# Performance work log

Measured on AMD Instinct MI355X. Metric: run time of the kernel, lower is better.

Reference implementation:

```python
import jax, jax.numpy as jnp
import numpy as np

GAMMA = 0.99
BETA = 0.01
B, T, A = 65536, 128, 8


def setup_inputs() -> dict:
    key = jax.random.key(0)
    ks = jax.random.split(key, 6)
    return {
        "values": jax.random.normal(ks[0], (B, T), jnp.float32),
        "last_value": jax.random.normal(ks[1], (B,), jnp.float32),
        "rewards": jax.random.normal(ks[2], (B, T), jnp.float32),
        "log_probs": -jax.nn.softplus(jax.random.normal(ks[3], (B, T, A), jnp.float32)),
        "entropies": jax.random.uniform(ks[4], (B, T, A), jnp.float32),
        "terminal_mask": jax.random.randint(ks[5], (B,), 0, 2) > 0,
    }


def _a3c_loss(values, last_value, rewards, log_probs, entropies, terminal_mask):
    # Bootstrap value R: zero if terminal, else detached last-state value
    R0 = jnp.where(terminal_mask, 0.0, jax.lax.stop_gradient(last_value))  # [B]
    values_next = jnp.concatenate([values[:, 1:], R0[:, None]], axis=1)    # [B,T] = values[i+1]
    lp = log_probs.sum(-1)    # [B,T], log_probs[i].sum()
    ent = entropies.sum(-1)   # [B,T], entropies[i].sum()

    # scan over time (reverse), xs laid out time-major: [T, B]
    xs = (rewards.T, values.T, values_next.T, lp.T, ent.T)
    z = jnp.zeros((values.shape[0],), values.dtype)

    def step(carry, x):
        R, gae, actor, critic = carry
        r, v, v_next, l, e = x
        R = GAMMA * R + r
        adv = R - v
        critic = critic + 0.5 * adv * adv
        delta = r + GAMMA * v_next - v
        gae = gae * GAMMA + delta
        actor = actor - l * jax.lax.stop_gradient(gae) - BETA * e
        return (R, gae, actor, critic), None

    (R, gae, actor, critic), _ = jax.lax.scan(step, (R0, z, z, z), xs, reverse=True)
    return jnp.stack([actor, critic], axis=-1)  # [B, 2]: (actor_loss, critic_loss)


def reference(values, last_value, rewards, log_probs, entropies, terminal_mask):
    return _a3c_loss(values, last_value, rewards, log_probs, entropies, terminal_mask)
```

## Files before the change

kernel.cpp:

```cpp
#include <hip/hip_runtime.h>

#define GAMMA 0.99f
#define BETA  0.01f

__global__ __launch_bounds__(256, 8) void a3c_loss_kernel(
    const float* __restrict__ values,
    const float* __restrict__ last_value,
    const float* __restrict__ rewards,
    const float* __restrict__ log_probs,
    const float* __restrict__ entropies,
    const int*   __restrict__ terminal_mask,
    float* __restrict__ out,
    int B)
{
    const int wave = threadIdx.x >> 6;
    const int lane = threadIdx.x & 63;
    const int b = blockIdx.x * 4 + wave;
    if (b >= B) return;

    const float2 v2 = reinterpret_cast<const float2*>(values  + (size_t)b * 128)[lane];
    const float2 r2 = reinterpret_cast<const float2*>(rewards + (size_t)b * 128)[lane];
    const float4* lp4 = reinterpret_cast<const float4*>(log_probs + (size_t)b * 1024) + lane * 4;
    const float4* en4 = reinterpret_cast<const float4*>(entropies + (size_t)b * 1024) + lane * 4;
    const float4 la = lp4[0], lb = lp4[1], lc = lp4[2], ld = lp4[3];
    const float4 ea = en4[0], eb = en4[1], ec = en4[2], ed = en4[3];

    const float v0 = v2.x, v1 = v2.y;
    const float r0 = r2.x, r1 = r2.y;
    const float lp0 = (la.x + la.y + la.z + la.w) + (lb.x + lb.y + lb.z + lb.w);
    const float lp1 = (lc.x + lc.y + lc.z + lc.w) + (ld.x + ld.y + ld.z + ld.w);
    const float esum = (ea.x + ea.y + ea.z + ea.w) + (eb.x + eb.y + eb.z + eb.w)
                     + (ec.x + ec.y + ec.z + ec.w) + (ed.x + ed.y + ed.z + ed.w);

    const float R0 = (terminal_mask[b] != 0) ? 0.0f : last_value[b];

    float vnext1 = __shfl_down(v0, 1, 64);
    if (lane == 63) vnext1 = R0;
    const float delta1 = r1 + GAMMA * vnext1 - v1;
    const float delta0 = r0 + GAMMA * v1    - v0;

    float m  = GAMMA * GAMMA;
    float cR = fmaf(GAMMA, r1, r0);
    float cG = fmaf(GAMMA, delta1, delta0);

    #pragma unroll
    for (int d = 1; d < 64; d <<= 1) {
        const float om  = __shfl_down(m,  d, 64);
        const float ocR = __shfl_down(cR, d, 64);
        const float ocG = __shfl_down(cG, d, 64);
        if (lane + d < 64) {
            cR = fmaf(m, ocR, cR);
            cG = fmaf(m, ocG, cG);
            m  = m * om;
        }
    }
    float pm  = __shfl_down(m,  1, 64);
    float pcR = __shfl_down(cR, 1, 64);
    float pcG = __shfl_down(cG, 1, 64);
    if (lane == 63) { pm = 1.0f; pcR = 0.0f; pcG = 0.0f; }

    const float Rin = fmaf(pm, R0, pcR);
    const float gin = pcG;

    const float R1   = fmaf(GAMMA, Rin, r1);
    const float Rt0  = fmaf(GAMMA, R1,  r0);
    const float adv1 = R1  - v1;
    const float adv0 = Rt0 - v0;
    float critic = 0.5f * (adv1 * adv1 + adv0 * adv0);

    const float g1 = fmaf(GAMMA, gin, delta1);
    const float g0 = fmaf(GAMMA, g1,  delta0);
    float actor = -(lp1 * g1 + lp0 * g0) - BETA * esum;

    #pragma unroll
    for (int d = 32; d >= 1; d >>= 1) {
        actor  += __shfl_down(actor,  d, 64);
        critic += __shfl_down(critic, d, 64);
    }

    if (lane == 0) {
        reinterpret_cast<float2*>(out)[b] = make_float2(actor, critic);
    }
}

extern "C" void kernel_launch(void* const* d_in, const int* in_sizes, int n_in,
                              void* d_out, int out_size, void* d_ws, size_t ws_size,
                              hipStream_t stream) {
    const float* values      = (const float*)d_in[0];
    const float* last_value  = (const float*)d_in[1];
    const float* rewards     = (const float*)d_in[2];
    const float* log_probs   = (const float*)d_in[3];
    const float* entropies   = (const float*)d_in[4];
    const int*   terminal    = (const int*)d_in[5];
    float* out = (float*)d_out;

    const int B = in_sizes[1];
    const int blocks = (B + 3) / 4;

    a3c_loss_kernel<<<blocks, 256, 0, stream>>>(
        values, last_value, rewards, log_probs, entropies, terminal, out, B);
}
```

Measured before the change: 540.4 us.

## Process multiple batch rows per wave with double-buffered loads and coalesced log-prob reads

Each wave now handles 8 batch rows, prefetching the next row's data into a second register set while computing the current one. The log_probs and entropies loads switch from per-lane contiguous 64-byte chunks to lane-strided float4 loads for full coalescing. The gae values are redistributed across lanes with shuffles to match the new layout. This raises memory-level parallelism and coalescing, at the cost of more registers, lower occupancy (launch bounds 4) and extra shuffles.

Result: no change. 539.3 us (-0.2%).

```diff
diff --git a/kernel.cpp b/kernel.cpp
--- a/kernel.cpp
+++ b/kernel.cpp
@@ -2,37 +2,42 @@
 
 #define GAMMA 0.99f
 #define BETA  0.01f
+#define NB 8
+#define WPB 4
 
-__global__ __launch_bounds__(256, 8) void a3c_loss_kernel(
-    const float* __restrict__ values,
-    const float* __restrict__ last_value,
-    const float* __restrict__ rewards,
-    const float* __restrict__ log_probs,
-    const float* __restrict__ entropies,
-    const int*   __restrict__ terminal_mask,
-    float* __restrict__ out,
-    int B)
+
+struct BatchRegs {
+    float2 v2, r2;
+    float  lv;
+    int    tm;
+    float4 L0, L1, L2, L3;
+    float4 E0, E1, E2, E3;
+};
+
+__device__ __forceinline__ void load_batch(
+    const float* __restrict__ values, const float* __restrict__ last_value,
+    const float* __restrict__ rewards, const float* __restrict__ log_probs,
+    const float* __restrict__ entropies, const int* __restrict__ terminal_mask,
+    int b, int lane, BatchRegs& S)
 {
-    const int wave = threadIdx.x >> 6;
-    const int lane = threadIdx.x & 63;
-    const int b = blockIdx.x * 4 + wave;
-    if (b >= B) return;
+    S.v2 = reinterpret_cast<const float2*>(values  + (size_t)b * 128)[lane];
+    S.r2 = reinterpret_cast<const float2*>(rewards + (size_t)b * 128)[lane];
+    S.lv = last_value[b];
+    S.tm = terminal_mask[b];
+    const float4* lp4 = reinterpret_cast<const float4*>(log_probs + (size_t)b * 1024);
+    const float4* en4 = reinterpret_cast<const float4*>(entropies + (size_t)b * 1024);
+    S.L0 = lp4[lane      ]; S.L1 = lp4[lane +  64];
+    S.L2 = lp4[lane + 128]; S.L3 = lp4[lane + 192];
+    S.E0 = en4[lane      ]; S.E1 = en4[lane +  64];
+    S.E2 = en4[lane + 128]; S.E3 = en4[lane + 192];
+}
 
-    const float2 v2 = reinterpret_cast<const float2*>(values  + (size_t)b * 128)[lane];
-    const float2 r2 = reinterpret_cast<const float2*>(rewards + (size_t)b * 128)[lane];
-    const float4* lp4 = reinterpret_cast<const float4*>(log_probs + (size_t)b * 1024) + lane * 4;
-    const float4* en4 = reinterpret_cast<const float4*>(entropies + (size_t)b * 1024) + lane * 4;
-    const float4 la = lp4[0], lb = lp4[1], lc = lp4[2], ld = lp4[3];
-    const float4 ea = en4[0], eb = en4[1], ec = en4[2], ed = en4[3];
-
-    const float v0 = v2.x, v1 = v2.y;
-    const float r0 = r2.x, r1 = r2.y;
-    const float lp0 = (la.x + la.y + la.z + la.w) + (lb.x + lb.y + lb.z + lb.w);
-    const float lp1 = (lc.x + lc.y + lc.z + lc.w) + (ld.x + ld.y + ld.z + ld.w);
-    const float esum = (ea.x + ea.y + ea.z + ea.w) + (eb.x + eb.y + eb.z + eb.w)
-                     + (ec.x + ec.y + ec.z + ec.w) + (ed.x + ed.y + ed.z + ed.w);
-
-    const float R0 = (terminal_mask[b] != 0) ? 0.0f : last_value[b];
+__device__ __forceinline__ void compute_store(
+    const BatchRegs& S, int lane, int b, float* __restrict__ out)
+{
+    const float v0 = S.v2.x, v1 = S.v2.y;
+    const float r0 = S.r2.x, r1 = S.r2.y;
+    const float R0 = (S.tm != 0) ? 0.0f : S.lv;
 
     float vnext1 = __shfl_down(v0, 1, 64);
     if (lane == 63) vnext1 = R0;
@@ -70,16 +75,70 @@
 
     const float g1 = fmaf(GAMMA, gin, delta1);
     const float g0 = fmaf(GAMMA, g1,  delta0);
-    float actor = -(lp1 * g1 + lp0 * g0) - BETA * esum;
+
+    const int par = (lane >> 1) & 1;
+    const int hb  = lane >> 2;
+    const float gA0 = __shfl(g0, hb,      64), gB0 = __shfl(g1, hb,      64);
+    const float gA1 = __shfl(g0, hb + 16, 64), gB1 = __shfl(g1, hb + 16, 64);
+    const float gA2 = __shfl(g0, hb + 32, 64), gB2 = __shfl(g1, hb + 32, 64);
+    const float gA3 = __shfl(g0, hb + 48, 64), gB3 = __shfl(g1, hb + 48, 64);
+    const float gk0 = par ? gB0 : gA0;
+    const float gk1 = par ? gB1 : gA1;
+    const float gk2 = par ? gB2 : gA2;
+    const float gk3 = par ? gB3 : gA3;
+    const float sL0 = (S.L0.x + S.L0.y) + (S.L0.z + S.L0.w);
+    const float sL1 = (S.L1.x + S.L1.y) + (S.L1.z + S.L1.w);
+    const float sL2 = (S.L2.x + S.L2.y) + (S.L2.z + S.L2.w);
+    const float sL3 = (S.L3.x + S.L3.y) + (S.L3.z + S.L3.w);
+    float actor = -(sL0 * gk0 + sL1 * gk1 + sL2 * gk2 + sL3 * gk3);
+
+    const float esum =
+          ((S.E0.x + S.E0.y) + (S.E0.z + S.E0.w)) + ((S.E1.x + S.E1.y) + (S.E1.z + S.E1.w))
+        + ((S.E2.x + S.E2.y) + (S.E2.z + S.E2.w)) + ((S.E3.x + S.E3.y) + (S.E3.z + S.E3.w));
+    actor = fmaf(-BETA, esum, actor);
 
     #pragma unroll
     for (int d = 32; d >= 1; d >>= 1) {
         actor  += __shfl_down(actor,  d, 64);
         critic += __shfl_down(critic, d, 64);
     }
-
     if (lane == 0) {
         reinterpret_cast<float2*>(out)[b] = make_float2(actor, critic);
+    }
+}
+
+__global__ __launch_bounds__(256, 4) void a3c_loss_kernel(
+    const float* __restrict__ values,
+    const float* __restrict__ last_value,
+    const float* __restrict__ rewards,
+    const float* __restrict__ log_probs,
+    const float* __restrict__ entropies,
+    const int*   __restrict__ terminal_mask,
+    float* __restrict__ out,
+    int B)
+{
+    const int wave = threadIdx.x >> 6;
+    const int lane = threadIdx.x & 63;
+    const int b0 = (blockIdx.x * WPB + wave) * NB;
+    if (b0 >= B) return;
+
+    BatchRegs Ra, Rb;
+    load_batch(values, last_value, rewards, log_probs, entropies, terminal_mask,
+               b0, lane, Ra);
+
+    #pragma unroll
+    for (int i = 0; i < NB; i += 2) {
+        const int bi = b0 + i;
+        if (i + 1 < NB && bi + 1 < B)
+            load_batch(values, last_value, rewards, log_probs, entropies,
+                       terminal_mask, bi + 1, lane, Rb);
+        compute_store(Ra, lane, bi, out);
+        if (i + 1 < NB && bi + 1 < B) {
+            if (i + 2 < NB && bi + 2 < B)
+                load_batch(values, last_value, rewards, log_probs, entropies,
+                           terminal_mask, bi + 2, lane, Ra);
+            compute_store(Rb, lane, bi + 1, out);
+        }
     }
 }
 
@@ -95,7 +154,7 @@
     float* out = (float*)d_out;
 
     const int B = in_sizes[1];
-    const int blocks = (B + 3) / 4;
+    const int blocks = (B + WPB * NB - 1) / (WPB * NB);
 
     a3c_loss_kernel<<<blocks, 256, 0, stream>>>(
         values, last_value, rewards, log_probs, entropies, terminal, out, B);
```
